# Optimization experiments

Hardware: AMD Instinct MI355X
Metric: run time of the kernel (lower is better)

The kernel has to match this reference:

```python
import jax, jax.numpy as jnp
import numpy as np

B, N, D, E = 2, 50000, 128, 640000


def setup_inputs() -> dict:
    key = jax.random.key(0)
    ks = jax.random.split(key, 7)
    x = jax.random.normal(ks[0], (B, N, D), dtype=jnp.float32)
    edge_index = jax.random.randint(ks[1], (2, E), 0, N)
    edge_attr = jax.random.uniform(ks[2], (E,), dtype=jnp.float32)
    s = 1.0 / np.sqrt(D)
    W1 = jax.random.uniform(ks[3], (D, D), jnp.float32, -s, s)
    b1 = jax.random.uniform(ks[4], (D,), jnp.float32, -s, s)
    W2 = jax.random.uniform(ks[5], (D, D), jnp.float32, -s, s)
    b2 = jax.random.uniform(ks[6], (D,), jnp.float32, -s, s)
    return {"x": x, "edge_index": edge_index, "edge_attr": edge_attr,
            "W1": W1, "b1": b1, "W2": W2, "b2": b2}


def _gcn_layer(x, W, b, row, col, norm, n):
    # x: [B, N, D] -> transform then gather-scale-scatter along edges
    h = jnp.einsum('bnd,df->bnf', x, W)
    msg = h[:, row, :] * norm[None, :, None]          # [B, E2, D]
    agg = jax.vmap(lambda m: jax.ops.segment_sum(m, col, num_segments=n))(msg)
    return agg + b


def reference(x, edge_index, edge_attr, W1, b1, W2, b2):
    n = x.shape[1]
    row, col = edge_index[0], edge_index[1]
    # GCNConv default: add self loops (weight 1), symmetric normalization
    loop = jnp.arange(n)
    row2 = jnp.concatenate([row, loop])
    col2 = jnp.concatenate([col, loop])
    w2 = jnp.concatenate([edge_attr, jnp.ones((n,), edge_attr.dtype)])
    deg = jax.ops.segment_sum(w2, col2, num_segments=n)
    dinv = jnp.where(deg > 0, jax.lax.rsqrt(deg), 0.0)
    norm = dinv[row2] * w2 * dinv[col2]               # [E2]
    # dropout is identity in eval mode
    h = jax.nn.relu(_gcn_layer(x, W1, b1, row2, col2, norm, n))
    h = jax.nn.relu(_gcn_layer(h, W2, b2, row2, col2, norm, n))
    return h
```

## Files before the change

### kernel.cpp

```cpp
#include <hip/hip_runtime.h>

#define NNODES 50000
#define NBATCH 2
#define DIM    128
#define NEDGE  640000
#define M_TOT  (NBATCH*NNODES)

typedef unsigned short u16;
typedef unsigned int   u32;

typedef __attribute__((ext_vector_type(8))) short bf16x8;
typedef __attribute__((ext_vector_type(4))) float f32x4;

__device__ __forceinline__ float bf2f(u16 u){ return __uint_as_float(((u32)u)<<16); }
__device__ __forceinline__ u16 f2bf(float f){
    u32 x = __float_as_uint(f);
    x += 0x7fffu + ((x>>16)&1u);
    return (u16)(x>>16);
}


__global__ __launch_bounds__(256) void init_k(float* deg, int* cnt, int* fill){
    int i = blockIdx.x*256 + threadIdx.x;
    if (i < NNODES){ deg[i] = 1.0f; cnt[i] = 0; fill[i] = 0; }
}

__global__ __launch_bounds__(256) void count_k(const int* __restrict__ ei,
                                               const float* __restrict__ ea,
                                               float* deg, int* cnt){
    int e = blockIdx.x*256 + threadIdx.x;
    if (e < NEDGE){
        int c = ei[NEDGE + e];
        atomicAdd(&deg[c], ea[e]);
        atomicAdd(&cnt[c], 1);
    }
}

__global__ __launch_bounds__(256) void scan1(const int* __restrict__ cnt,
                                             int* colstart, int* bsum,
                                             const float* __restrict__ deg,
                                             float* __restrict__ dinv){
    __shared__ int s[256];
    int tid = threadIdx.x;
    int i = blockIdx.x*256 + tid;
    if (i < NNODES){ float d = deg[i]; dinv[i] = (d > 0.f) ? rsqrtf(d) : 0.f; }
    int v = (i < NNODES) ? cnt[i] : 0;
    s[tid] = v; __syncthreads();
    #pragma unroll
    for (int off = 1; off < 256; off <<= 1){
        int t = (tid >= off) ? s[tid-off] : 0;
        __syncthreads();
        s[tid] += t;
        __syncthreads();
    }
    if (i < NNODES) colstart[i] = s[tid] - v;
    if (tid == 255) bsum[blockIdx.x] = s[255];
}

__global__ __launch_bounds__(256) void scan2(int* bsum, int nb){
    __shared__ int s[256];
    int tid = threadIdx.x;
    int v = (tid < nb) ? bsum[tid] : 0;
    s[tid] = v; __syncthreads();
    #pragma unroll
    for (int off = 1; off < 256; off <<= 1){
        int t = (tid >= off) ? s[tid-off] : 0;
        __syncthreads();
        s[tid] += t;
        __syncthreads();
    }
    if (tid < nb) bsum[tid] = s[tid] - v;
}

__global__ __launch_bounds__(256) void scan3(int* colstart, const int* bsum){
    int i = blockIdx.x*256 + threadIdx.x;
    if (i < NNODES) colstart[i] += bsum[i >> 8];
}

__global__ __launch_bounds__(256) void fill_k(const int* __restrict__ ei,
                                              const float* __restrict__ ea,
                                              const float* __restrict__ dinv,
                                              const int* __restrict__ colstart,
                                              int* fill, int2* __restrict__ epack){
    int e = blockIdx.x*256 + threadIdx.x;
    if (e < NEDGE){
        int r = ei[e], c = ei[NEDGE + e];
        int pos = colstart[c] + atomicAdd(&fill[c], 1);
        epack[pos] = make_int2(r, __float_as_int(dinv[r] * ea[e] * dinv[c]));
    }
}

__global__ __launch_bounds__(256) void transposeW(const float* __restrict__ W1, u16* __restrict__ Wt1,
                                                  const float* __restrict__ W2, u16* __restrict__ Wt2){
    int i = blockIdx.x*256 + threadIdx.x;
    const float* W = (i < 16384) ? W1 : W2;
    u16* Wt       = (i < 16384) ? Wt1 : Wt2;
    int ii = i & 16383;
    int k = ii >> 7, n = ii & 127;
    Wt[n*DIM + k] = f2bf(W[ii]);
}

__device__ __forceinline__ bf16x8 load_frag(const float* A, size_t off){
    const float4* ap = (const float4*)(A + off);
    float4 lo = ap[0], hi = ap[1];
    bf16x8 r;
    r[0] = (short)f2bf(lo.x); r[1] = (short)f2bf(lo.y);
    r[2] = (short)f2bf(lo.z); r[3] = (short)f2bf(lo.w);
    r[4] = (short)f2bf(hi.x); r[5] = (short)f2bf(hi.y);
    r[6] = (short)f2bf(hi.z); r[7] = (short)f2bf(hi.w);
    return r;
}
__device__ __forceinline__ bf16x8 load_frag(const u16* A, size_t off){
    return *(const bf16x8*)(A + off);
}

template <typename AT>
__global__ __launch_bounds__(256) void gemm128(const AT* __restrict__ A,
                                               const u16* __restrict__ Wt,
                                               u16* __restrict__ H, int M){
    __shared__ u16 Wl[128][136];
    int tid = threadIdx.x;
    {
        const uint4* src = (const uint4*)Wt;
        #pragma unroll
        for (int j = 0; j < 8; ++j){
            int g = tid + j*256;
            int n = g >> 4;
            int k = (g & 15) * 8;
            *(uint4*)&Wl[n][k] = src[g];
        }
    }
    __syncthreads();

    int wave = tid >> 6, lane = tid & 63;
    int quad = lane >> 4, r = lane & 15;
    int row0 = blockIdx.x*256 + wave*64;

    f32x4 acc[4][8];
    #pragma unroll
    for (int mt = 0; mt < 4; ++mt)
        #pragma unroll
        for (int nt = 0; nt < 8; ++nt)
            acc[mt][nt] = (f32x4){0.f,0.f,0.f,0.f};

    #pragma unroll
    for (int ks = 0; ks < 4; ++ks){
        bf16x8 af[4];
        #pragma unroll
        for (int mt = 0; mt < 4; ++mt){
            int row = row0 + mt*16 + r;
            if (row < M)
                af[mt] = load_frag(A, (size_t)row*DIM + ks*32 + quad*8);
            else
                af[mt] = (bf16x8){0,0,0,0,0,0,0,0};
        }
        #pragma unroll
        for (int nt = 0; nt < 8; ++nt){
            bf16x8 bfr = *(const bf16x8*)&Wl[nt*16 + r][ks*32 + quad*8];
            #pragma unroll
            for (int mt = 0; mt < 4; ++mt)
                acc[mt][nt] = __builtin_amdgcn_mfma_f32_16x16x32_bf16(af[mt], bfr, acc[mt][nt], 0, 0, 0);
        }
    }

    #pragma unroll
    for (int mt = 0; mt < 4; ++mt){
        #pragma unroll
        for (int reg = 0; reg < 4; ++reg){
            int row = row0 + mt*16 + quad*4 + reg;
            if (row < M){
                #pragma unroll
                for (int nt = 0; nt < 8; ++nt)
                    H[(size_t)row*DIM + nt*16 + r] = f2bf(acc[mt][nt][reg]);
            }
        }
    }
}

#define EDGE_FMA(W_, V0_, V1_)                                            \
    a0 = fmaf(W_, bf2f((u16)((V0_) & 0xffff)), a0);                       \
    a1 = fmaf(W_, bf2f((u16)((V0_) >> 16)),    a1);                       \
    a2 = fmaf(W_, bf2f((u16)((V1_) & 0xffff)), a2);                       \
    a3 = fmaf(W_, bf2f((u16)((V1_) >> 16)),    a3);

template <bool OUT_F32>
__global__ __launch_bounds__(256) void gather2_k(const u16* __restrict__ H,
                                                 const int2* __restrict__ epack,
                                                 const int* __restrict__ colstart,
                                                 const int* __restrict__ cnt,
                                                 const float* __restrict__ dinv,
                                                 const float* __restrict__ bias,
                                                 void* __restrict__ out){
    int wave = threadIdx.x >> 6, lane = threadIdx.x & 63;
    int n = blockIdx.x*4 + wave;
    if (n >= NNODES) return;
    const u32* H0 = (const u32*)H;
    const u32* H1 = H0 + (size_t)NNODES*64;

    float dn = dinv[n], dn2 = dn*dn;
    u32 sv0 = H0[(size_t)n*64 + lane];
    u32 sv1 = H1[(size_t)n*64 + lane];
    float a0 = dn2*bf2f((u16)(sv0 & 0xffff)), a1 = dn2*bf2f((u16)(sv0 >> 16));
    float a2 = dn2*bf2f((u16)(sv1 & 0xffff)), a3 = dn2*bf2f((u16)(sv1 >> 16));

    int s = colstart[n], c = cnt[n];
    for (int base = 0; base < c; base += 64){
        int m = min(64, c - base);
        int2 ep = make_int2(0, 0);
        if (lane < m) ep = epack[s + base + lane];
        int j = 0;
        for (; j + 4 <= m; j += 4){
            int   r0 = __shfl(ep.x, j+0), r1 = __shfl(ep.x, j+1);
            int   r2 = __shfl(ep.x, j+2), r3 = __shfl(ep.x, j+3);
            float w0 = __int_as_float(__shfl(ep.y, j+0));
            float w1 = __int_as_float(__shfl(ep.y, j+1));
            float w2 = __int_as_float(__shfl(ep.y, j+2));
            float w3 = __int_as_float(__shfl(ep.y, j+3));
            u32 v00 = H0[(size_t)r0*64 + lane], v10 = H1[(size_t)r0*64 + lane];
            u32 v01 = H0[(size_t)r1*64 + lane], v11 = H1[(size_t)r1*64 + lane];
            u32 v02 = H0[(size_t)r2*64 + lane], v12 = H1[(size_t)r2*64 + lane];
            u32 v03 = H0[(size_t)r3*64 + lane], v13 = H1[(size_t)r3*64 + lane];
            EDGE_FMA(w0, v00, v10)
            EDGE_FMA(w1, v01, v11)
            EDGE_FMA(w2, v02, v12)
            EDGE_FMA(w3, v03, v13)
        }
        for (; j < m; ++j){
            int   rr = __shfl(ep.x, j);
            float ww = __int_as_float(__shfl(ep.y, j));
            u32 v0 = H0[(size_t)rr*64 + lane], v1 = H1[(size_t)rr*64 + lane];
            EDGE_FMA(ww, v0, v1)
        }
    }
    float bb0 = bias[lane*2], bb1 = bias[lane*2 + 1];
    a0 = fmaxf(a0 + bb0, 0.f); a1 = fmaxf(a1 + bb1, 0.f);
    a2 = fmaxf(a2 + bb0, 0.f); a3 = fmaxf(a3 + bb1, 0.f);
    if (OUT_F32){
        float2* O = (float2*)out;
        O[(size_t)n*64 + lane]            = make_float2(a0, a1);
        O[(size_t)(NNODES + n)*64 + lane] = make_float2(a2, a3);
    } else {
        u32* O = (u32*)out;
        O[(size_t)n*64 + lane]            = (u32)f2bf(a0) | ((u32)f2bf(a1) << 16);
        O[(size_t)(NNODES + n)*64 + lane] = (u32)f2bf(a2) | ((u32)f2bf(a3) << 16);
    }
}

extern "C" void kernel_launch(void* const* d_in, const int* in_sizes, int n_in,
                              void* d_out, int out_size, void* d_ws, size_t ws_size,
                              hipStream_t stream){
    const float* x  = (const float*)d_in[0];
    const int*   ei = (const int*)  d_in[1];
    const float* ea = (const float*)d_in[2];
    const float* W1 = (const float*)d_in[3];
    const float* b1 = (const float*)d_in[4];
    const float* W2 = (const float*)d_in[5];
    const float* b2 = (const float*)d_in[6];

    char* p = (char*)d_ws;
    auto alloc = [&](size_t bytes)->char*{ char* r = p; p += (bytes + 511) & ~(size_t)511; return r; };
    float* deg      = (float*)alloc(NNODES*4);
    float* dinv     = (float*)alloc(NNODES*4);
    int*   cnt      = (int*)  alloc(NNODES*4);
    int*   colstart = (int*)  alloc(NNODES*4);
    int*   fill     = (int*)  alloc(NNODES*4);
    int*   bsum     = (int*)  alloc(1024);
    int2*  epack    = (int2*) alloc((size_t)NEDGE*8);
    u16*   Wt1      = (u16*)  alloc(DIM*DIM*2);
    u16*   Wt2      = (u16*)  alloc(DIM*DIM*2);
    u16*   h        = (u16*)  alloc((size_t)M_TOT*DIM*2);
    u16*   o1       = (u16*)  alloc((size_t)M_TOT*DIM*2);

    const int NBL_N = (NNODES + 255)/256;
    const int NBL_E = (NEDGE  + 255)/256;
    const int NTILE = (M_TOT + 255)/256;
    const int NBL_G = (NNODES + 3)/4;

    transposeW<<<128, 256, 0, stream>>>(W1, Wt1, W2, Wt2);
    init_k <<<NBL_N, 256, 0, stream>>>(deg, cnt, fill);
    count_k<<<NBL_E, 256, 0, stream>>>(ei, ea, deg, cnt);
    scan1  <<<NBL_N, 256, 0, stream>>>(cnt, colstart, bsum, deg, dinv);
    scan2  <<<1,     256, 0, stream>>>(bsum, NBL_N);
    scan3  <<<NBL_N, 256, 0, stream>>>(colstart, bsum);
    fill_k <<<NBL_E, 256, 0, stream>>>(ei, ea, dinv, colstart, fill, epack);

    gemm128<float><<<NTILE, 256, 0, stream>>>(x, Wt1, h, M_TOT);
    gather2_k<false><<<NBL_G, 256, 0, stream>>>(h, epack, colstart, cnt, dinv, b1, o1);
    gemm128<u16>  <<<NTILE, 256, 0, stream>>>(o1, Wt2, h, M_TOT);
    gather2_k<true> <<<NBL_G, 256, 0, stream>>>(h, epack, colstart, cnt, dinv, b2, d_out);
}
```

Before: 331.9 us.

## Use per-XCD packed 64-bit atomics for degree/count and precomputed CSR ranks

Replaces the two global atomics per edge (float degree and int count) with a single 64-bit atomic into a per-XCD partial array that packs a fixed-point weight sum with the count, at workgroup scope. The returned old value gives each edge its rank within its XCD partition, so the fill pass no longer needs a second atomic. scan1 combines the eight partitions into counts, per-partition offsets and dinv. The goal is less contention and less cross-XCD coherence traffic in CSR construction. The risks are fixed-point rounding of the degree, workgroup-scope atomics relying on XCC_ID register semantics, and a 16-bit per-partition rank limit.

```diff
diff --git a/kernel.cpp b/kernel.cpp
--- a/kernel.cpp
+++ b/kernel.cpp
@@ -5,9 +5,11 @@
 #define DIM    128
 #define NEDGE  640000
 #define M_TOT  (NBATCH*NNODES)
+#define NXCD   8
 
 typedef unsigned short u16;
 typedef unsigned int   u32;
+typedef unsigned long long u64;
 
 typedef __attribute__((ext_vector_type(8))) short bf16x8;
 typedef __attribute__((ext_vector_type(4))) float f32x4;
@@ -19,32 +21,44 @@
     return (u16)(x>>16);
 }
 
-
-__global__ __launch_bounds__(256) void init_k(float* deg, int* cnt, int* fill){
-    int i = blockIdx.x*256 + threadIdx.x;
-    if (i < NNODES){ deg[i] = 1.0f; cnt[i] = 0; fill[i] = 0; }
-}
-
 __global__ __launch_bounds__(256) void count_k(const int* __restrict__ ei,
                                                const float* __restrict__ ea,
-                                               float* deg, int* cnt){
+                                               u64* __restrict__ part,
+                                               u32* __restrict__ rankpack){
+    u32 xcc = __builtin_amdgcn_s_getreg(6164) & 7u;
     int e = blockIdx.x*256 + threadIdx.x;
     if (e < NEDGE){
         int c = ei[NEDGE + e];
-        atomicAdd(&deg[c], ea[e]);
-        atomicAdd(&cnt[c], 1);
-    }
-}
-
-__global__ __launch_bounds__(256) void scan1(const int* __restrict__ cnt,
-                                             int* colstart, int* bsum,
-                                             const float* __restrict__ deg,
-                                             float* __restrict__ dinv){
+        u64 inc = (((u64)__float2uint_rn(ea[e] * 16777216.0f)) << 32) | 1ull;
+        u64 old = __hip_atomic_fetch_add(&part[(size_t)xcc*NNODES + c], inc,
+                                         __ATOMIC_RELAXED, __HIP_MEMORY_SCOPE_WORKGROUP);
+        rankpack[e] = ((u32)old & 0xffffu) | (xcc << 16);
+    }
+}
+
+__global__ __launch_bounds__(256) void scan1(const u64* __restrict__ part,
+                                             int* __restrict__ cnt,
+                                             int* __restrict__ poff,
+                                             float* __restrict__ dinv,
+                                             int* colstart, int* bsum){
     __shared__ int s[256];
     int tid = threadIdx.x;
-    int i = blockIdx.x*256 + tid;
-    if (i < NNODES){ float d = deg[i]; dinv[i] = (d > 0.f) ? rsqrtf(d) : 0.f; }
-    int v = (i < NNODES) ? cnt[i] : 0;
+    int n = blockIdx.x*256 + tid;
+    int v = 0;
+    if (n < NNODES){
+        int run = 0; u64 fsum = 0;
+        #pragma unroll
+        for (int p = 0; p < NXCD; ++p){
+            u64 pv = part[(size_t)p*NNODES + n];
+            poff[p*NNODES + n] = run;
+            run  += (int)(pv & 0xffffffffu);
+            fsum += (pv >> 32);
+        }
+        cnt[n] = run;
+        v = run;
+        float deg = 1.0f + (float)fsum * (1.0f/16777216.0f);
+        dinv[n] = rsqrtf(deg);
+    }
     s[tid] = v; __syncthreads();
     #pragma unroll
     for (int off = 1; off < 256; off <<= 1){
@@ -53,7 +67,7 @@
         s[tid] += t;
         __syncthreads();
     }
-    if (i < NNODES) colstart[i] = s[tid] - v;
+    if (n < NNODES) colstart[n] = s[tid] - v;
     if (tid == 255) bsum[blockIdx.x] = s[255];
 }
 
@@ -81,11 +95,14 @@
                                               const float* __restrict__ ea,
                                               const float* __restrict__ dinv,
                                               const int* __restrict__ colstart,
-                                              int* fill, int2* __restrict__ epack){
+                                              const int* __restrict__ poff,
+                                              const u32* __restrict__ rankpack,
+                                              int2* __restrict__ epack){
     int e = blockIdx.x*256 + threadIdx.x;
     if (e < NEDGE){
         int r = ei[e], c = ei[NEDGE + e];
-        int pos = colstart[c] + atomicAdd(&fill[c], 1);
+        u32 rp = rankpack[e];
+        int pos = colstart[c] + poff[(rp >> 16)*NNODES + c] + (int)(rp & 0xffffu);
         epack[pos] = make_int2(r, __float_as_int(dinv[r] * ea[e] * dinv[c]));
     }
 }
@@ -259,11 +276,12 @@
 
     char* p = (char*)d_ws;
     auto alloc = [&](size_t bytes)->char*{ char* r = p; p += (bytes + 511) & ~(size_t)511; return r; };
-    float* deg      = (float*)alloc(NNODES*4);
+    u64*   part     = (u64*)  alloc((size_t)NXCD*NNODES*8);
+    u32*   rankpack = (u32*)  alloc((size_t)NEDGE*4);
+    int*   poff     = (int*)  alloc((size_t)NXCD*NNODES*4);
     float* dinv     = (float*)alloc(NNODES*4);
     int*   cnt      = (int*)  alloc(NNODES*4);
     int*   colstart = (int*)  alloc(NNODES*4);
-    int*   fill     = (int*)  alloc(NNODES*4);
     int*   bsum     = (int*)  alloc(1024);
     int2*  epack    = (int2*) alloc((size_t)NEDGE*8);
     u16*   Wt1      = (u16*)  alloc(DIM*DIM*2);
@@ -276,13 +294,13 @@
     const int NTILE = (M_TOT + 255)/256;
     const int NBL_G = (NNODES + 3)/4;
 
+    hipMemsetAsync(part, 0, (size_t)NXCD*NNODES*8, stream);
     transposeW<<<128, 256, 0, stream>>>(W1, Wt1, W2, Wt2);
-    init_k <<<NBL_N, 256, 0, stream>>>(deg, cnt, fill);
-    count_k<<<NBL_E, 256, 0, stream>>>(ei, ea, deg, cnt);
-    scan1  <<<NBL_N, 256, 0, stream>>>(cnt, colstart, bsum, deg, dinv);
+    count_k<<<NBL_E, 256, 0, stream>>>(ei, ea, part, rankpack);
+    scan1  <<<NBL_N, 256, 0, stream>>>(part, cnt, poff, dinv, colstart, bsum);
     scan2  <<<1,     256, 0, stream>>>(bsum, NBL_N);
     scan3  <<<NBL_N, 256, 0, stream>>>(colstart, bsum);
-    fill_k <<<NBL_E, 256, 0, stream>>>(ei, ea, dinv, colstart, fill, epack);
+    fill_k <<<NBL_E, 256, 0, stream>>>(ei, ea, dinv, colstart, poff, rankpack, epack);
 
     gemm128<float><<<NTILE, 256, 0, stream>>>(x, Wt1, h, M_TOT);
     gather2_k<false><<<NBL_G, 256, 0, stream>>>(h, epack, colstart, cnt, dinv, b1, o1);
```

New measurement: 286.3 us. 1.16x faster.
